# Performance work log

Measured on AMD Instinct MI355X. Metric: run time of the kernel, lower is better.

## Reference

```python
import jax, jax.numpy as jnp
import numpy as np

P_DIM, M_DIM = 512, 768
PROJ, HID, NCLS = 512, 256, 2
EPS = 1e-5


def _bn_eval(x, g, b):
    # BatchNorm1d in eval mode with fresh buffers: running_mean=0, running_var=1
    return x / jnp.sqrt(1.0 + EPS) * g + b


def setup_inputs() -> dict:
    key = jax.random.key(0)
    ks = jax.random.split(key, 8)
    x = jax.random.normal(ks[0], (256, P_DIM + M_DIM), dtype=jnp.float32)
    W1 = jax.random.normal(ks[1], (PROJ, P_DIM * M_DIM), dtype=jnp.float32) * 0.002
    b1 = jnp.zeros((PROJ,), jnp.float32)
    ln_g = jnp.ones((PROJ,), jnp.float32)
    ln_b = jnp.zeros((PROJ,), jnp.float32)
    W2 = jax.random.normal(ks[2], (HID, PROJ), dtype=jnp.float32) * 0.04
    b2 = jnp.zeros((HID,), jnp.float32)
    bn1_g = jnp.ones((HID,), jnp.float32)
    bn1_b = jnp.zeros((HID,), jnp.float32)
    W3 = jax.random.normal(ks[3], (HID // 2, HID), dtype=jnp.float32) * 0.06
    b3 = jnp.zeros((HID // 2,), jnp.float32)
    bn2_g = jnp.ones((HID // 2,), jnp.float32)
    bn2_b = jnp.zeros((HID // 2,), jnp.float32)
    W4 = jax.random.normal(ks[4], (NCLS, HID // 2), dtype=jnp.float32) * 0.09
    b4 = jnp.zeros((NCLS,), jnp.float32)
    return dict(x=x, W1=W1, b1=b1, ln_g=ln_g, ln_b=ln_b, W2=W2, b2=b2,
                bn1_g=bn1_g, bn1_b=bn1_b, W3=W3, b3=b3,
                bn2_g=bn2_g, bn2_b=bn2_b, W4=W4, b4=b4)


def reference(x, W1, b1, ln_g, ln_b, W2, b2, bn1_g, bn1_b, W3, b3, bn2_g, bn2_b, W4, b4):
    p = x[:, :P_DIM]                     # [B, P]
    m = x[:, P_DIM:P_DIM + M_DIM]        # [B, M]
    # kron[b, i*M + j] = p[b,i]*m[b,j]; Linear(kron_flat) fused into one contraction
    W1r = W1.reshape(PROJ, P_DIM, M_DIM)
    fused = jnp.einsum('bp,bm,kpm->bk', p, m, W1r) + b1   # [B, PROJ]
    # LayerNorm + ReLU (dropout is identity in eval)
    mu = jnp.mean(fused, axis=-1, keepdims=True)
    var = jnp.var(fused, axis=-1, keepdims=True)
    h = (fused - mu) / jnp.sqrt(var + EPS) * ln_g + ln_b
    h = jax.nn.relu(h)
    # classifier MLP with BatchNorm1d (eval-mode buffers)
    h = jax.nn.relu(_bn_eval(h @ W2.T + b2, bn1_g, bn1_b))
    h = jax.nn.relu(_bn_eval(h @ W3.T + b3, bn2_g, bn2_b))
    logits = h @ W4.T + b4               # [B, NCLS]
    return logits
```

## Files before the change

kernel.cpp:

```cpp
#include <hip/hip_runtime.h>
#include <hip/hip_bf16.h>

typedef __attribute__((ext_vector_type(4))) float f32x4;
typedef __attribute__((ext_vector_type(16))) float f32x16;
typedef __attribute__((ext_vector_type(8))) short short8;
typedef unsigned short ushort_t;

#define BATCH 256
#define PDIM 512
#define MDIM 768
#define XCOLS 1280
#define PROJ 512
#define HID 256
#define KTOT (PDIM * MDIM)

#define BN 32
#define NT 16
#define PSPLIT 64
#define PI_PER 8
#define NJW 12
#define NSTEPS 96

__device__ __forceinline__ ushort_t f2bf(float f) {
  __hip_bfloat16 h = __float2bfloat16(f);
  return __builtin_bit_cast(ushort_t, h);
}
__device__ __forceinline__ float bf2f(ushort_t u) {
  union { unsigned int i; float f; } c;
  c.i = ((unsigned int)u) << 16;
  return c.f;
}

__global__ void prep_kernel(const float* __restrict__ x, float* __restrict__ pT,
                            ushort_t* __restrict__ mF) {
  int tid = blockIdx.x * blockDim.x + threadIdx.x;
  int nth = gridDim.x * blockDim.x;
  for (int i = tid; i < PDIM * BATCH; i += nth) {
    int pi = i >> 8, b = i & 255;
    pT[i] = x[b * XCOLS + pi];
  }
  for (int c = tid; c < NJW * 8 * 4 * 64; c += nth) {
    int lane = c & 63;
    int ks = (c >> 6) & 3;
    int mf = (c >> 8) & 7;
    int jw = c >> 11;
    int row = mf * 32 + (lane & 31);
    int k0 = jw * 64 + ks * 16 + ((lane >> 5) << 3);
    const float* src = x + row * XCOLS + PDIM + k0;
    f32x4 v0 = *(const f32x4*)src;
    f32x4 v1 = *(const f32x4*)(src + 4);
    short8 o;
#pragma unroll
    for (int i = 0; i < 4; ++i) {
      o[i] = (short)f2bf(v0[i]);
      o[i + 4] = (short)f2bf(v1[i]);
    }
    ((short8*)mF)[c] = o;
  }
}

__global__ __launch_bounds__(256, 4)
void einsum_kernel(const float* __restrict__ W1, const ushort_t* __restrict__ mF,
                   const float* __restrict__ pT, float* __restrict__ outp,
                   int atomic_mode) {
  __shared__ ushort_t Bf[2][2048];
  __shared__ float pl[PI_PER * BATCH];

  const int ntile = blockIdx.x & 15;
  const int ps    = blockIdx.x >> 4;
  const int pi0   = ps * PI_PER;
  const int n0    = ntile * BN;
  const int t     = threadIdx.x;
  const int lane  = t & 63;
  const int w     = t >> 6;

  {
    const f32x4* src = (const f32x4*)(pT + pi0 * BATCH);
    ((f32x4*)pl)[t] = src[t];
    ((f32x4*)pl)[t + 256] = src[t + 256];
  }

  const int sn = t >> 3, q = t & 7;
  const float* wbase = W1 + (size_t)(n0 + sn) * KTOT + (size_t)pi0 * MDIM + q * 8;
  const int bwo = (((q >> 1) * 64) + ((q & 1) << 5) + sn) * 8;

  const short8* mv = (const short8*)mF;
  const int mbase = w * 512 + lane;
  short8 ac0 = mv[mbase];
  short8 ac1 = mv[mbase + 64];
  short8 ac2 = mv[mbase + 128];
  short8 ac3 = mv[mbase + 192];
  short8 ac4 = mv[mbase + 256];
  short8 ac5 = mv[mbase + 320];
  short8 ac6 = mv[mbase + 384];
  short8 ac7 = mv[mbase + 448];

  f32x4 wv0 = *(const f32x4*)(wbase);
  f32x4 wv1 = *(const f32x4*)(wbase + 4);

  f32x16 fa0, fa1;
#pragma unroll
  for (int i = 0; i < 16; ++i) { fa0[i] = 0.f; fa1[i] = 0.f; }

  __syncthreads();

  int koff = 0, pil = 0, jw = 0;

  for (int s = 0; s < NSTEPS; ++s) {
    const int nk = (pil < 7) ? (koff + MDIM) : (koff - 7 * MDIM + 64);
    f32x4 nv0 = *(const f32x4*)(wbase + nk);
    f32x4 nv1 = *(const f32x4*)(wbase + nk + 4);

    {
      short8 bs;
#pragma unroll
      for (int i = 0; i < 4; ++i) {
        bs[i]     = (short)f2bf(wv0[i]);
        bs[i + 4] = (short)f2bf(wv1[i]);
      }
      *(short8*)&Bf[s & 1][bwo] = bs;
    }
    asm volatile("s_waitcnt lgkmcnt(0)" ::: "memory");
    __builtin_amdgcn_s_barrier();
    asm volatile("" ::: "memory");

    const short8* bf = (const short8*)Bf[s & 1];
    short8 bv0 = bf[lane];
    short8 bv1 = bf[lane + 64];
    short8 bv2 = bf[lane + 128];
    short8 bv3 = bf[lane + 192];
    const float pa = pl[pil * BATCH + w * 64 + (lane & 31)];
    const float pb = pl[pil * BATCH + w * 64 + 32 + (lane & 31)];

#define GENMM(acA, acB, bv)                                          \
    {                                                                \
      short8 aA, aB;                                                 \
      _Pragma("unroll")                                              \
      for (int e = 0; e < 8; ++e) {                                  \
        aA[e] = (short)f2bf(pa * bf2f((ushort_t)acA[e]));            \
        aB[e] = (short)f2bf(pb * bf2f((ushort_t)acB[e]));            \
      }                                                              \
      fa0 = __builtin_amdgcn_mfma_f32_32x32x16_bf16(aA, bv, fa0, 0, 0, 0); \
      fa1 = __builtin_amdgcn_mfma_f32_32x32x16_bf16(aB, bv, fa1, 0, 0, 0); \
    }
    GENMM(ac0, ac4, bv0)
    GENMM(ac1, ac5, bv1)
    GENMM(ac2, ac6, bv2)
    GENMM(ac3, ac7, bv3)
#undef GENMM

    if (pil == 7) {
      const int jn = (jw + 1 == NJW) ? 0 : jw + 1;
      const short8* srcn = mv + jn * 2048;
      ac0 = srcn[mbase];
      ac1 = srcn[mbase + 64];
      ac2 = srcn[mbase + 128];
      ac3 = srcn[mbase + 192];
      ac4 = srcn[mbase + 256];
      ac5 = srcn[mbase + 320];
      ac6 = srcn[mbase + 384];
      ac7 = srcn[mbase + 448];
    }

    wv0 = nv0; wv1 = nv1; koff = nk;
    if (++pil == 8) { pil = 0; ++jw; }
  }

  const int col   = n0 + (lane & 31);
  const int rbase = w * 64 + ((lane >> 5) << 2);
  if (atomic_mode) {
#pragma unroll
    for (int r = 0; r < 16; ++r) {
      int row = rbase + (r & 3) + ((r >> 2) << 3);
      atomicAdd(&outp[(size_t)row * PROJ + col], fa0[r]);
      atomicAdd(&outp[(size_t)(row + 32) * PROJ + col], fa1[r]);
    }
  } else {
    float* dst = outp + (size_t)ps * BATCH * PROJ;
#pragma unroll
    for (int r = 0; r < 16; ++r) {
      int row = rbase + (r & 3) + ((r >> 2) << 3);
      dst[(size_t)row * PROJ + col] = fa0[r];
      dst[(size_t)(row + 32) * PROJ + col] = fa1[r];
    }
  }
}

__global__ __launch_bounds__(256)
void mlp_kernel(const float* __restrict__ part, int nps,
                const float* __restrict__ b1, const float* __restrict__ lng,
                const float* __restrict__ lnb, const float* __restrict__ W2,
                const float* __restrict__ b2, const float* __restrict__ g1,
                const float* __restrict__ bb1, const float* __restrict__ W3,
                const float* __restrict__ b3, const float* __restrict__ g2,
                const float* __restrict__ bb2, const float* __restrict__ W4,
                const float* __restrict__ b4, float* __restrict__ out) {
  __shared__ float h1[PROJ];
  __shared__ float h2[HID];
  __shared__ float h3[HID / 2];
  __shared__ float red[16];
  const int b = blockIdx.x, t = threadIdx.x;

  float f0 = 0.f, f1 = 0.f;
  const float* p0 = part + (size_t)b * PROJ + t;
#pragma unroll 4
  for (int s = 0; s < nps; ++s) {
    f0 += p0[0];
    f1 += p0[256];
    p0 += (size_t)BATCH * PROJ;
  }
  f0 += b1[t];
  f1 += b1[t + 256];

  float sum = f0 + f1, ss = f0 * f0 + f1 * f1;
#pragma unroll
  for (int o = 32; o > 0; o >>= 1) {
    sum += __shfl_xor(sum, o);
    ss  += __shfl_xor(ss, o);
  }
  const int wv = t >> 6, ln = t & 63;
  if (ln == 0) { red[wv] = sum; red[8 + wv] = ss; }
  __syncthreads();
  sum = red[0] + red[1] + red[2] + red[3];
  ss  = red[8] + red[9] + red[10] + red[11];
  float mu   = sum * (1.f / 512.f);
  float var  = ss * (1.f / 512.f) - mu * mu;
  float rstd = rsqrtf(var + 1e-5f);
  h1[t]       = fmaxf(0.f, (f0 - mu) * rstd * lng[t] + lnb[t]);
  h1[t + 256] = fmaxf(0.f, (f1 - mu) * rstd * lng[t + 256] + lnb[t + 256]);
  __syncthreads();

  const float bninv = rsqrtf(1.f + 1e-5f);
  {
    const f32x4* wr = (const f32x4*)(W2 + (size_t)t * PROJ);
    const f32x4* hv = (const f32x4*)h1;
    float a = 0.f;
#pragma unroll 4
    for (int i = 0; i < PROJ / 4; ++i) {
      f32x4 wq = wr[i], h = hv[i];
      a += wq[0] * h[0] + wq[1] * h[1] + wq[2] * h[2] + wq[3] * h[3];
    }
    h2[t] = fmaxf(0.f, (a + b2[t]) * bninv * g1[t] + bb1[t]);
  }
  __syncthreads();
  if (t < 128) {
    const f32x4* wr = (const f32x4*)(W3 + (size_t)t * HID);
    const f32x4* hv = (const f32x4*)h2;
    float a = 0.f;
#pragma unroll 4
    for (int i = 0; i < HID / 4; ++i) {
      f32x4 wq = wr[i], h = hv[i];
      a += wq[0] * h[0] + wq[1] * h[1] + wq[2] * h[2] + wq[3] * h[3];
    }
    h3[t] = fmaxf(0.f, (a + b3[t]) * bninv * g2[t] + bb2[t]);
  }
  __syncthreads();
  if (t < 2) {
    const float* wr = W4 + t * 128;
    float a = 0.f;
#pragma unroll 4
    for (int i = 0; i < 128; ++i) a += wr[i] * h3[i];
    out[b * 2 + t] = a + b4[t];
  }
}

extern "C" void kernel_launch(void* const* d_in, const int* in_sizes, int n_in,
                              void* d_out, int out_size, void* d_ws, size_t ws_size,
                              hipStream_t stream) {
  const float* x   = (const float*)d_in[0];
  const float* W1  = (const float*)d_in[1];
  const float* b1  = (const float*)d_in[2];
  const float* lng = (const float*)d_in[3];
  const float* lnb = (const float*)d_in[4];
  const float* W2  = (const float*)d_in[5];
  const float* b2  = (const float*)d_in[6];
  const float* g1  = (const float*)d_in[7];
  const float* bb1 = (const float*)d_in[8];
  const float* W3  = (const float*)d_in[9];
  const float* b3  = (const float*)d_in[10];
  const float* g2  = (const float*)d_in[11];
  const float* bb2 = (const float*)d_in[12];
  const float* W4  = (const float*)d_in[13];
  const float* b4  = (const float*)d_in[14];
  float* out = (float*)d_out;

  char* ws = (char*)d_ws;
  float* pT    = (float*)ws;
  ushort_t* mF = (ushort_t*)(ws + 524288);
  float* big   = (float*)(ws + 1048576);

  size_t need = 1048576 + (size_t)PSPLIT * BATCH * PROJ * 4;
  bool partial = ws_size >= need;

  hipLaunchKernelGGL(prep_kernel, dim3(512), dim3(256), 0, stream, x, pT, mF);
  if (partial) {
    hipLaunchKernelGGL(einsum_kernel, dim3(NT * PSPLIT), dim3(256), 0, stream,
                       W1, mF, pT, big, 0);
    hipLaunchKernelGGL(mlp_kernel, dim3(BATCH), dim3(256), 0, stream, big, PSPLIT,
                       b1, lng, lnb, W2, b2, g1, bb1, W3, b3, g2, bb2, W4, b4, out);
  } else {
    hipMemsetAsync(big, 0, (size_t)BATCH * PROJ * 4, stream);
    hipLaunchKernelGGL(einsum_kernel, dim3(NT * PSPLIT), dim3(256), 0, stream,
                       W1, mF, pT, big, 1);
    hipLaunchKernelGGL(mlp_kernel, dim3(BATCH), dim3(256), 0, stream, big, 1,
                       b1, lng, lnb, W2, b2, g1, bb1, W3, b3, g2, bb2, W4, b4, out);
  }
}
```

Before: 237.7 us.

## Stagger per-block W1 traversal, prefetch two steps ahead with nontemporal loads

Each block now starts its walk over the (pil, jw) W1 tiles at a hashed offset, so concurrent blocks touch different DRAM regions and channels instead of all hitting the same offsets in lockstep. W1 loads move from one step ahead to two steps ahead, and use nontemporal loads because W1 is streamed once. Launch bounds drop from 4 to 3 waves-per-EU to leave register room for the extra in-flight buffers. The change trades some occupancy and extra index math for better latency hiding and more even memory-channel use.

```diff
diff --git a/kernel.cpp b/kernel.cpp
--- a/kernel.cpp
+++ b/kernel.cpp
@@ -59,7 +59,7 @@
   }
 }
 
-__global__ __launch_bounds__(256, 4)
+__global__ __launch_bounds__(256, 3)
 void einsum_kernel(const float* __restrict__ W1, const ushort_t* __restrict__ mF,
                    const float* __restrict__ pT, float* __restrict__ outp,
                    int atomic_mode) {
@@ -74,6 +74,10 @@
   const int lane  = t & 63;
   const int w     = t >> 6;
 
+  const unsigned hsh = blockIdx.x * 2654435761u;
+  const int pil0 = (hsh >> 8) & 7;
+  const int jw0  = (int)((((hsh >> 16) & 0xffff) * 12u) >> 16);
+
   {
     const f32x4* src = (const f32x4*)(pT + pi0 * BATCH);
     ((f32x4*)pl)[t] = src[t];
@@ -84,19 +88,34 @@
   const float* wbase = W1 + (size_t)(n0 + sn) * KTOT + (size_t)pi0 * MDIM + q * 8;
   const int bwo = (((q >> 1) * 64) + ((q & 1) << 5) + sn) * 8;
 
+  auto koff = [&](int tt) {
+    int pil = (pil0 + (tt & 7)) & 7;
+    int g = jw0 + (tt >> 3);
+    if (g >= NJW) g -= NJW;
+    return pil * MDIM + g * 64;
+  };
+
   const short8* mv = (const short8*)mF;
   const int mbase = w * 512 + lane;
-  short8 ac0 = mv[mbase];
-  short8 ac1 = mv[mbase + 64];
-  short8 ac2 = mv[mbase + 128];
-  short8 ac3 = mv[mbase + 192];
-  short8 ac4 = mv[mbase + 256];
-  short8 ac5 = mv[mbase + 320];
-  short8 ac6 = mv[mbase + 384];
-  short8 ac7 = mv[mbase + 448];
-
-  f32x4 wv0 = *(const f32x4*)(wbase);
-  f32x4 wv1 = *(const f32x4*)(wbase + 4);
+  const short8* srcA = mv + jw0 * 2048;
+  short8 ac0 = srcA[mbase];
+  short8 ac1 = srcA[mbase + 64];
+  short8 ac2 = srcA[mbase + 128];
+  short8 ac3 = srcA[mbase + 192];
+  short8 ac4 = srcA[mbase + 256];
+  short8 ac5 = srcA[mbase + 320];
+  short8 ac6 = srcA[mbase + 384];
+  short8 ac7 = srcA[mbase + 448];
+
+  f32x4 wv0, wv1, nv0, nv1;
+  {
+    const float* p0 = wbase + koff(0);
+    wv0 = __builtin_nontemporal_load((const f32x4*)p0);
+    wv1 = __builtin_nontemporal_load((const f32x4*)(p0 + 4));
+    const float* p1 = wbase + koff(1);
+    nv0 = __builtin_nontemporal_load((const f32x4*)p1);
+    nv1 = __builtin_nontemporal_load((const f32x4*)(p1 + 4));
+  }
 
   f32x16 fa0, fa1;
 #pragma unroll
@@ -104,12 +123,11 @@
 
   __syncthreads();
 
-  int koff = 0, pil = 0, jw = 0;
-
   for (int s = 0; s < NSTEPS; ++s) {
-    const int nk = (pil < 7) ? (koff + MDIM) : (koff - 7 * MDIM + 64);
-    f32x4 nv0 = *(const f32x4*)(wbase + nk);
-    f32x4 nv1 = *(const f32x4*)(wbase + nk + 4);
+    int t2 = s + 2; t2 = (t2 >= NSTEPS) ? t2 - NSTEPS : t2;
+    const float* wp2 = wbase + koff(t2);
+    f32x4 xv0 = __builtin_nontemporal_load((const f32x4*)wp2);
+    f32x4 xv1 = __builtin_nontemporal_load((const f32x4*)(wp2 + 4));
 
     {
       short8 bs;
@@ -129,8 +147,9 @@
     short8 bv1 = bf[lane + 64];
     short8 bv2 = bf[lane + 128];
     short8 bv3 = bf[lane + 192];
-    const float pa = pl[pil * BATCH + w * 64 + (lane & 31)];
-    const float pb = pl[pil * BATCH + w * 64 + 32 + (lane & 31)];
+    const int pilc = (pil0 + (s & 7)) & 7;
+    const float pa = pl[pilc * BATCH + w * 64 + (lane & 31)];
+    const float pb = pl[pilc * BATCH + w * 64 + 32 + (lane & 31)];
 
 #define GENMM(acA, acB, bv)                                          \
     {                                                                \
@@ -149,9 +168,10 @@
     GENMM(ac3, ac7, bv3)
 #undef GENMM
 
-    if (pil == 7) {
-      const int jn = (jw + 1 == NJW) ? 0 : jw + 1;
-      const short8* srcn = mv + jn * 2048;
+    if ((s & 7) == 7) {
+      int g = jw0 + ((s + 1) >> 3);
+      if (g >= NJW) g -= NJW;
+      const short8* srcn = mv + g * 2048;
       ac0 = srcn[mbase];
       ac1 = srcn[mbase + 64];
       ac2 = srcn[mbase + 128];
@@ -162,8 +182,8 @@
       ac7 = srcn[mbase + 448];
     }
 
-    wv0 = nv0; wv1 = nv1; koff = nk;
-    if (++pil == 8) { pil = 0; ++jw; }
+    wv0 = nv0; wv1 = nv1;
+    nv0 = xv0; nv1 = xv1;
   }
 
   const int col   = n0 + (lane & 31);
```

Measured after the change: 240.7 us. About the same (+1.3%).

## Coalesce W1 streaming loads, swizzle LDS B tile, and drop the pT transpose

Applied to the files above, without the earlier changes.

Each group of 8 threads now reads one W1 row as two fully contiguous 128-byte segments using nontemporal loads, instead of per-thread 32-byte chunks. The bf16 B tile is stored in LDS with an XOR swizzle so the MFMA operand reads avoid bank conflicts. The p operand is loaded straight from x into shared memory, which removes the transpose pass and its workspace buffer from the prep kernel. The loop also drops a redundant barrier and simplifies its index arithmetic. The goal is better HBM efficiency on the very large W1 stream, but the swizzle indexing must exactly match the MFMA operand layout.

```diff
diff --git a/kernel.cpp b/kernel.cpp
--- a/kernel.cpp
+++ b/kernel.cpp
@@ -4,6 +4,7 @@
 typedef __attribute__((ext_vector_type(4))) float f32x4;
 typedef __attribute__((ext_vector_type(16))) float f32x16;
 typedef __attribute__((ext_vector_type(8))) short short8;
+typedef __attribute__((ext_vector_type(4))) short short4v;
 typedef unsigned short ushort_t;
 
 #define BATCH 256
@@ -31,14 +32,9 @@
   return c.f;
 }
 
-__global__ void prep_kernel(const float* __restrict__ x, float* __restrict__ pT,
-                            ushort_t* __restrict__ mF) {
+__global__ void prep_kernel(const float* __restrict__ x, ushort_t* __restrict__ mF) {
   int tid = blockIdx.x * blockDim.x + threadIdx.x;
   int nth = gridDim.x * blockDim.x;
-  for (int i = tid; i < PDIM * BATCH; i += nth) {
-    int pi = i >> 8, b = i & 255;
-    pT[i] = x[b * XCOLS + pi];
-  }
   for (int c = tid; c < NJW * 8 * 4 * 64; c += nth) {
     int lane = c & 63;
     int ks = (c >> 6) & 3;
@@ -61,7 +57,7 @@
 
 __global__ __launch_bounds__(256, 4)
 void einsum_kernel(const float* __restrict__ W1, const ushort_t* __restrict__ mF,
-                   const float* __restrict__ pT, float* __restrict__ outp,
+                   const float* __restrict__ x, float* __restrict__ outp,
                    int atomic_mode) {
   __shared__ ushort_t Bf[2][2048];
   __shared__ float pl[PI_PER * BATCH];
@@ -75,14 +71,25 @@
   const int w     = t >> 6;
 
   {
-    const f32x4* src = (const f32x4*)(pT + pi0 * BATCH);
-    ((f32x4*)pl)[t] = src[t];
-    ((f32x4*)pl)[t + 256] = src[t + 256];
-  }
-
-  const int sn = t >> 3, q = t & 7;
-  const float* wbase = W1 + (size_t)(n0 + sn) * KTOT + (size_t)pi0 * MDIM + q * 8;
-  const int bwo = (((q >> 1) * 64) + ((q & 1) << 5) + sn) * 8;
+    const float* xr = x + (size_t)t * XCOLS + pi0;
+    f32x4 v0 = *(const f32x4*)xr;
+    f32x4 v1 = *(const f32x4*)(xr + 4);
+    pl[t]             = v0[0];
+    pl[256 + t]       = v0[1];
+    pl[512 + t]       = v0[2];
+    pl[768 + t]       = v0[3];
+    pl[1024 + t]      = v1[0];
+    pl[1280 + t]      = v1[1];
+    pl[1536 + t]      = v1[2];
+    pl[1792 + t]      = v1[3];
+  }
+
+  const int r = t >> 3, q = t & 7;
+  const float* wrow = W1 + (size_t)(n0 + r) * KTOT + (size_t)pi0 * MDIM;
+  const int wb0 = (r * 128 + q * 8) ^ ((r & 7) << 4);
+  const int wb1 = (r * 128 + 64 + q * 8) ^ ((r & 7) << 4);
+
+  const int bb0 = ((lane & 31) * 128 + ((lane >> 5) << 4)) ^ ((lane & 7) << 4);
 
   const short8* mv = (const short8*)mF;
   const int mbase = w * 512 + lane;
@@ -95,42 +102,42 @@
   short8 ac6 = mv[mbase + 384];
   short8 ac7 = mv[mbase + 448];
 
-  f32x4 wv0 = *(const f32x4*)(wbase);
-  f32x4 wv1 = *(const f32x4*)(wbase + 4);
+  f32x4 wv0 = __builtin_nontemporal_load((const f32x4*)(wrow + q * 4));
+  f32x4 wv1 = __builtin_nontemporal_load((const f32x4*)(wrow + 32 + q * 4));
 
   f32x16 fa0, fa1;
 #pragma unroll
   for (int i = 0; i < 16; ++i) { fa0[i] = 0.f; fa1[i] = 0.f; }
 
-  __syncthreads();
-
-  int koff = 0, pil = 0, jw = 0;
-
   for (int s = 0; s < NSTEPS; ++s) {
-    const int nk = (pil < 7) ? (koff + MDIM) : (koff - 7 * MDIM + 64);
-    f32x4 nv0 = *(const f32x4*)(wbase + nk);
-    f32x4 nv1 = *(const f32x4*)(wbase + nk + 4);
+    const int s1 = (s + 1 < NSTEPS) ? s + 1 : 0;
+    const int kk1 = (s1 & 7) * MDIM + (s1 >> 3) * 64;
+    f32x4 nv0 = __builtin_nontemporal_load((const f32x4*)(wrow + kk1 + q * 4));
+    f32x4 nv1 = __builtin_nontemporal_load((const f32x4*)(wrow + kk1 + 32 + q * 4));
 
     {
-      short8 bs;
+      short4v lo, hi;
 #pragma unroll
       for (int i = 0; i < 4; ++i) {
-        bs[i]     = (short)f2bf(wv0[i]);
-        bs[i + 4] = (short)f2bf(wv1[i]);
+        lo[i] = (short)f2bf(wv0[i]);
+        hi[i] = (short)f2bf(wv1[i]);
       }
-      *(short8*)&Bf[s & 1][bwo] = bs;
+      char* bbase = (char*)&Bf[s & 1][0];
+      *(short4v*)(bbase + wb0) = lo;
+      *(short4v*)(bbase + wb1) = hi;
     }
     asm volatile("s_waitcnt lgkmcnt(0)" ::: "memory");
     __builtin_amdgcn_s_barrier();
     asm volatile("" ::: "memory");
 
-    const short8* bf = (const short8*)Bf[s & 1];
-    short8 bv0 = bf[lane];
-    short8 bv1 = bf[lane + 64];
-    short8 bv2 = bf[lane + 128];
-    short8 bv3 = bf[lane + 192];
-    const float pa = pl[pil * BATCH + w * 64 + (lane & 31)];
-    const float pb = pl[pil * BATCH + w * 64 + 32 + (lane & 31)];
+    const char* rb = (const char*)&Bf[s & 1][0];
+    short8 bv0 = *(const short8*)(rb + (bb0 ^ 0));
+    short8 bv1 = *(const short8*)(rb + (bb0 ^ 32));
+    short8 bv2 = *(const short8*)(rb + (bb0 ^ 64));
+    short8 bv3 = *(const short8*)(rb + (bb0 ^ 96));
+    const int pilc = s & 7;
+    const float pa = pl[pilc * BATCH + w * 64 + (lane & 31)];
+    const float pb = pl[pilc * BATCH + w * 64 + 32 + (lane & 31)];
 
 #define GENMM(acA, acB, bv)                                          \
     {                                                                \
@@ -149,8 +156,9 @@
     GENMM(ac3, ac7, bv3)
 #undef GENMM
 
-    if (pil == 7) {
-      const int jn = (jw + 1 == NJW) ? 0 : jw + 1;
+    if ((s & 7) == 7) {
+      int jn = (s >> 3) + 1;
+      if (jn >= NJW) jn = 0;
       const short8* srcn = mv + jn * 2048;
       ac0 = srcn[mbase];
       ac1 = srcn[mbase + 64];
@@ -162,26 +170,25 @@
       ac7 = srcn[mbase + 448];
     }
 
-    wv0 = nv0; wv1 = nv1; koff = nk;
-    if (++pil == 8) { pil = 0; ++jw; }
+    wv0 = nv0; wv1 = nv1;
   }
 
   const int col   = n0 + (lane & 31);
   const int rbase = w * 64 + ((lane >> 5) << 2);
   if (atomic_mode) {
 #pragma unroll
-    for (int r = 0; r < 16; ++r) {
-      int row = rbase + (r & 3) + ((r >> 2) << 3);
-      atomicAdd(&outp[(size_t)row * PROJ + col], fa0[r]);
-      atomicAdd(&outp[(size_t)(row + 32) * PROJ + col], fa1[r]);
+    for (int rr = 0; rr < 16; ++rr) {
+      int row = rbase + (rr & 3) + ((rr >> 2) << 3);
+      atomicAdd(&outp[(size_t)row * PROJ + col], fa0[rr]);
+      atomicAdd(&outp[(size_t)(row + 32) * PROJ + col], fa1[rr]);
     }
   } else {
     float* dst = outp + (size_t)ps * BATCH * PROJ;
 #pragma unroll
-    for (int r = 0; r < 16; ++r) {
-      int row = rbase + (r & 3) + ((r >> 2) << 3);
-      dst[(size_t)row * PROJ + col] = fa0[r];
-      dst[(size_t)(row + 32) * PROJ + col] = fa1[r];
+    for (int rr = 0; rr < 16; ++rr) {
+      int row = rbase + (rr & 3) + ((rr >> 2) << 3);
+      dst[(size_t)row * PROJ + col] = fa0[rr];
+      dst[(size_t)(row + 32) * PROJ + col] = fa1[rr];
     }
   }
 }
@@ -285,23 +292,22 @@
   float* out = (float*)d_out;
 
   char* ws = (char*)d_ws;
-  float* pT    = (float*)ws;
-  ushort_t* mF = (ushort_t*)(ws + 524288);
-  float* big   = (float*)(ws + 1048576);
-
-  size_t need = 1048576 + (size_t)PSPLIT * BATCH * PROJ * 4;
+  ushort_t* mF = (ushort_t*)ws;
+  float* big   = (float*)(ws + 524288);
+
+  size_t need = 524288 + (size_t)PSPLIT * BATCH * PROJ * 4;
   bool partial = ws_size >= need;
 
-  hipLaunchKernelGGL(prep_kernel, dim3(512), dim3(256), 0, stream, x, pT, mF);
+  hipLaunchKernelGGL(prep_kernel, dim3(256), dim3(256), 0, stream, x, mF);
   if (partial) {
     hipLaunchKernelGGL(einsum_kernel, dim3(NT * PSPLIT), dim3(256), 0, stream,
-                       W1, mF, pT, big, 0);
+                       W1, mF, x, big, 0);
     hipLaunchKernelGGL(mlp_kernel, dim3(BATCH), dim3(256), 0, stream, big, PSPLIT,
                        b1, lng, lnb, W2, b2, g1, bb1, W3, b3, g2, bb2, W4, b4, out);
   } else {
     hipMemsetAsync(big, 0, (size_t)BATCH * PROJ * 4, stream);
     hipLaunchKernelGGL(einsum_kernel, dim3(NT * PSPLIT), dim3(256), 0, stream,
-                       W1, mF, pT, big, 1);
+                       W1, mF, x, big, 1);
     hipLaunchKernelGGL(mlp_kernel, dim3(BATCH), dim3(256), 0, stream, big, 1,
                        b1, lng, lnb, W2, b2, g1, bb1, W3, b3, g2, bb2, W4, b4, out);
   }
```

New measurement: 226.1 us. 4.9% less time.
